# Optimization experiments

Measured on AMD Instinct MI355X. Metric: run time of the kernel, lower is better.

The kernel has to match this reference:

```python
import jax, jax.numpy as jnp
import numpy as np

T = 0.07          # cfg.CAP.TEMP
K = 50            # cfg.CAP.HARD_NEG_K
LOSS_WEIGHT = 0.5 # cfg.CAP.LOSS_WEIGHT
C_CAM = 8         # number of cameras
P = 2048          # pseudo-ID classes per camera bank


def setup_inputs() -> dict:
    key = jax.random.key(0)
    k1, k2, k3, k4 = jax.random.split(key, 4)
    B, D = 256, 2048
    inputs = jax.random.normal(k1, (B, D), jnp.float32)
    labels = jax.random.randint(k2, (B,), 0, P)
    cams = jax.random.randint(k3, (B,), 0, C_CAM)
    tempV = jax.random.normal(k4, (C_CAM * P, D), jnp.float32)
    tempV = tempV / jnp.linalg.norm(tempV, axis=1, keepdims=True)  # memory rows are L2-normalized
    return {"inputs": inputs, "labels": labels, "cams": cams, "tempV": tempV}


def _seg_mean_sum(vals, cams):
    # original loops over unique cams: loss += mean(vals within cam); empty cams contribute 0
    sums = jax.ops.segment_sum(vals, cams, num_segments=C_CAM)
    cnts = jax.ops.segment_sum(jnp.ones_like(vals), cams, num_segments=C_CAM)
    return jnp.sum(jnp.where(cnts > 0, sums / jnp.maximum(cnts, 1.0), 0.0))


def reference(inputs, labels, cams, tempV):
    B = inputs.shape[0]
    # cfg.CAP.NORM_FEAT
    x = inputs / jnp.linalg.norm(inputs, axis=1, keepdims=True)

    # one fused matmul against the concatenated memory; per-camera banks are contiguous P-slices
    all_logits = x @ tempV.T                      # [B, C_CAM*P]
    logits3 = all_logits.reshape(B, C_CAM, P)

    # ---- intra-camera loss: logits against the sample's own camera bank ----
    percam = jnp.take_along_axis(logits3, cams[:, None, None], axis=1)[:, 0, :] / T  # [B, P]
    lse_i = jax.scipy.special.logsumexp(percam, axis=1)
    ce = lse_i - jnp.take_along_axis(percam, labels[:, None], axis=1)[:, 0]
    loss_intra = _seg_mean_sum(ce, cams)

    # ---- inter-camera loss with hard-negative mining ----
    rows = jnp.arange(B)[:, None]
    # each ID has one centroid in every camera bank: positions label + P*cam
    ori_ind = labels[:, None] + P * jnp.arange(C_CAM)[None, :]        # [B, C_CAM]
    sims = all_logits.at[rows, ori_ind].set(-10000.0)                 # mask positives
    _, sel_ind = jax.lax.top_k(sims, K)                               # hard negatives (== sort[-K:])
    ori_logits = jnp.take_along_axis(all_logits, ori_ind, axis=1) / T  # [B, C_CAM]
    sel_logits = jnp.take_along_axis(all_logits, sel_ind, axis=1) / T  # [B, K]
    cat = jnp.concatenate([ori_logits, sel_logits], axis=1)            # [B, C_CAM+K]
    lse_c = jax.scipy.special.logsumexp(cat, axis=1)
    # target = 1/len(ori) on positives, 0 on negatives -> lse - mean(positive logits)
    loss_k = lse_c - jnp.mean(ori_logits, axis=1)
    loss_inter = LOSS_WEIGHT * _seg_mean_sum(loss_k, cams)

    return (loss_intra, loss_inter)
```

## Files before the change

### kernel.cpp

```cpp
#include <hip/hip_runtime.h>
#include <hip/hip_bf16.h>

#define BATCH 256
#define DIM   2048
#define NMEM  16384
#define PCLS  2048
#define CCAM  8
#define KSEL  50
#define T_INV 14.285714285714285714f
#define NBIN  4096

typedef __bf16 bf16x8 __attribute__((ext_vector_type(8)));
typedef float  f32x4  __attribute__((ext_vector_type(4)));

static __device__ __forceinline__ unsigned int f2bf(float f) {
  unsigned int u = __float_as_uint(f);
  return (u + 0x7FFFu + ((u >> 16) & 1u)) >> 16;
}
static __device__ __forceinline__ unsigned int pk2(float lo, float hi) {
  return f2bf(lo) | (f2bf(hi) << 16);
}
static __device__ __forceinline__ int binof(float v) {
  float bf = fmaf(v, 1950.4762f, 2048.0f);
  bf = fminf(fmaxf(bf, 0.0f), 4095.0f);
  return (int)bf;
}

__global__ __launch_bounds__(256) void norm_cast_kernel(
    const float* __restrict__ in, unsigned short* __restrict__ xb) {
  __shared__ float red[256];
  const int b = blockIdx.x, t = threadIdx.x;
  const float4* row = (const float4*)(in + (size_t)b * DIM);
  float4 a0 = row[t];
  float4 a1 = row[t + 256];
  float ss = a0.x*a0.x + a0.y*a0.y + a0.z*a0.z + a0.w*a0.w
           + a1.x*a1.x + a1.y*a1.y + a1.z*a1.z + a1.w*a1.w;
  red[t] = ss; __syncthreads();
  for (int s = 128; s > 0; s >>= 1) { if (t < s) red[t] += red[t + s]; __syncthreads(); }
  const float rn = rsqrtf(red[0]);
  ushort4 o0, o1;
  o0.x = (unsigned short)f2bf(a0.x*rn); o0.y = (unsigned short)f2bf(a0.y*rn);
  o0.z = (unsigned short)f2bf(a0.z*rn); o0.w = (unsigned short)f2bf(a0.w*rn);
  o1.x = (unsigned short)f2bf(a1.x*rn); o1.y = (unsigned short)f2bf(a1.y*rn);
  o1.z = (unsigned short)f2bf(a1.z*rn); o1.w = (unsigned short)f2bf(a1.w*rn);
  *(ushort4*)&xb[(size_t)b * DIM + t * 4]         = o0;
  *(ushort4*)&xb[(size_t)b * DIM + (t + 256) * 4] = o1;
}

#define BM 128
#define BN 64
#define BK 64
#define LDT 72

__global__ __launch_bounds__(256, 2) void gemm_kernel(
    const unsigned short* __restrict__ X,
    const float* __restrict__ V,
    float* __restrict__ C) {
  __shared__ unsigned short As[BM * LDT];
  __shared__ unsigned short Bs[BN * LDT];
  const int t  = threadIdx.x;
  const int m0 = blockIdx.x * BM;
  const int n0 = blockIdx.y * BN;
  const int lane = t & 63;
  const int w    = t >> 6;
  const int wm   = (w >> 1) * 64;
  const int wn   = (w & 1) * 32;

  f32x4 acc[4][2];
#pragma unroll
  for (int i = 0; i < 4; i++)
#pragma unroll
    for (int j = 0; j < 2; j++) acc[i][j] = (f32x4){0.f, 0.f, 0.f, 0.f};

  const int sr = t >> 1;
  const int sh = (t & 1) * 32;
  const int rb = t >> 2;
  const int cb = (t & 3) * 16;
  const unsigned short* Xp = X + (size_t)(m0 + sr) * DIM + sh;
  const float*          Vp = V + (size_t)(n0 + rb) * DIM + cb;

  uint4  a0 = *(const uint4*)Xp;
  uint4  a1 = *(const uint4*)(Xp + 8);
  uint4  a2 = *(const uint4*)(Xp + 16);
  uint4  a3 = *(const uint4*)(Xp + 24);
  float4 b0 = *(const float4*)Vp;
  float4 b1 = *(const float4*)(Vp + 4);
  float4 b2 = *(const float4*)(Vp + 8);
  float4 b3 = *(const float4*)(Vp + 12);

  const int fr = lane & 15;
  const int fk = (lane >> 4) * 8;

  for (int k0 = 0; k0 < DIM; k0 += BK) {
    __syncthreads();
    *(uint4*)&As[sr * LDT + sh]      = a0;
    *(uint4*)&As[sr * LDT + sh + 8]  = a1;
    *(uint4*)&As[sr * LDT + sh + 16] = a2;
    *(uint4*)&As[sr * LDT + sh + 24] = a3;
    uint4 p0, p1;
    p0.x = pk2(b0.x, b0.y); p0.y = pk2(b0.z, b0.w);
    p0.z = pk2(b1.x, b1.y); p0.w = pk2(b1.z, b1.w);
    p1.x = pk2(b2.x, b2.y); p1.y = pk2(b2.z, b2.w);
    p1.z = pk2(b3.x, b3.y); p1.w = pk2(b3.z, b3.w);
    *(uint4*)&Bs[rb * LDT + cb]     = p0;
    *(uint4*)&Bs[rb * LDT + cb + 8] = p1;
    __syncthreads();

    if (k0 + BK < DIM) {
      a0 = *(const uint4*)(Xp + k0 + BK);
      a1 = *(const uint4*)(Xp + k0 + BK + 8);
      a2 = *(const uint4*)(Xp + k0 + BK + 16);
      a3 = *(const uint4*)(Xp + k0 + BK + 24);
      b0 = *(const float4*)(Vp + k0 + BK);
      b1 = *(const float4*)(Vp + k0 + BK + 4);
      b2 = *(const float4*)(Vp + k0 + BK + 8);
      b3 = *(const float4*)(Vp + k0 + BK + 12);
    }

#pragma unroll
    for (int kk = 0; kk < BK; kk += 32) {
      bf16x8 aF[4], bF[2];
#pragma unroll
      for (int i = 0; i < 4; i++)
        aF[i] = *(const bf16x8*)&As[(wm + i * 16 + fr) * LDT + kk + fk];
#pragma unroll
      for (int j = 0; j < 2; j++)
        bF[j] = *(const bf16x8*)&Bs[(wn + j * 16 + fr) * LDT + kk + fk];
#pragma unroll
      for (int i = 0; i < 4; i++)
#pragma unroll
        for (int j = 0; j < 2; j++)
          acc[i][j] = __builtin_amdgcn_mfma_f32_16x16x32_bf16(aF[i], bF[j], acc[i][j], 0, 0, 0);
    }
  }

  const int cr = (lane >> 4) * 4;
  const int cc = lane & 15;
#pragma unroll
  for (int i = 0; i < 4; i++)
#pragma unroll
    for (int j = 0; j < 2; j++)
#pragma unroll
      for (int r = 0; r < 4; r++)
        C[(size_t)(m0 + wm + i * 16 + cr + r) * NMEM + (n0 + wn + j * 16 + cc)] =
            acc[i][j][r];
}

__global__ __launch_bounds__(256) void row_loss_kernel(
    const float* __restrict__ logits,
    const int* __restrict__ labels, const int* __restrict__ cams,
    float* __restrict__ ce_out, float* __restrict__ lossk_out) {
  __shared__ float vals[NMEM];
  __shared__ int   hist[NBIN];
  __shared__ float red[256];
  __shared__ int   pint[256];
  __shared__ float bl[512];
  __shared__ int   bcount;
  __shared__ int   bstar_s, cabove_s;

  const int b = blockIdx.x, t = threadIdx.x;
  const float4* src = (const float4*)(logits + (size_t)b * NMEM);
#pragma unroll
  for (int i = 0; i < 16; i++) ((float4*)vals)[t + 256 * i] = src[t + 256 * i];
#pragma unroll
  for (int i = 0; i < NBIN / 256; i++) hist[t + 256 * i] = 0;
  if (t == 0) bcount = 0;
  const int cam = cams[b], label = labels[b];
  __syncthreads();

  const int s0 = cam * PCLS;
  float S = 0.f;
#pragma unroll
  for (int i = 0; i < 8; i++) S += __expf(vals[s0 + t + 256 * i] * T_INV);
  red[t] = S; __syncthreads();
  for (int s = 128; s > 0; s >>= 1) { if (t < s) red[t] += red[t + s]; __syncthreads(); }
  float ov[CCAM]; float sumo = 0.f;
  if (t == 0) {
    ce_out[b] = logf(red[0]) - vals[s0 + label] * T_INV;
#pragma unroll
    for (int c = 0; c < CCAM; c++) { ov[c] = vals[c * PCLS + label]; sumo += ov[c]; }
  }
  __syncthreads();
  if (t < CCAM) vals[t * PCLS + label] = -1e30f;
  __syncthreads();

#pragma unroll
  for (int i = 0; i < 64; i++) {
    int bin = binof(vals[t + 256 * i]);
    atomicAdd(&hist[bin], 1);
  }
  __syncthreads();

  int ps = 0;
#pragma unroll
  for (int i = 0; i < 16; i++) ps += hist[t * 16 + i];
  pint[t] = ps; __syncthreads();
  if (t == 0) {
    int cum = 0, bstar = 0, cab = 0;
    for (int tc = 255; tc >= 0; tc--) {
      if (cum + pint[tc] >= KSEL) {
        for (int bi = tc * 16 + 15; bi >= tc * 16; bi--) {
          int h = hist[bi];
          if (cum + h >= KSEL) { bstar = bi; cab = cum; break; }
          cum += h;
        }
        break;
      }
      cum += pint[tc];
    }
    bstar_s = bstar; cabove_s = cab;
  }
  __syncthreads();
  const int bstar = bstar_s;

  float S2 = 0.f;
#pragma unroll
  for (int i = 0; i < 64; i++) {
    float v = vals[t + 256 * i];
    int bin = binof(v);
    if (bin > bstar) S2 += __expf(v * T_INV);
    else if (bin == bstar) {
      int p = atomicAdd(&bcount, 1);
      if (p < 512) bl[p] = v;
    }
  }
  red[t] = S2; __syncthreads();
  for (int s = 128; s > 0; s >>= 1) { if (t < s) red[t] += red[t + s]; __syncthreads(); }

  if (t == 0) {
    float S2tot = red[0];
    int need = KSEL - cabove_s;
    int bc = min(bcount, 512);
    for (int r = 0; r < need; r++) {
      float mx = -1e30f; int mi = 0;
      for (int i = 0; i < bc; i++) if (bl[i] > mx) { mx = bl[i]; mi = i; }
      S2tot += __expf(mx * T_INV);
      bl[mi] = -1e30f;
    }
#pragma unroll
    for (int c = 0; c < CCAM; c++) S2tot += __expf(ov[c] * T_INV);
    lossk_out[b] = logf(S2tot) - (sumo * T_INV) * (1.0f / CCAM);
  }
}

__global__ __launch_bounds__(256) void finalize_kernel(
    const float* __restrict__ ce, const float* __restrict__ lossk,
    const int* __restrict__ cams, float* __restrict__ out) {
  __shared__ float ce_s[BATCH], lk_s[BATCH];
  __shared__ int   cam_s[BATCH];
  __shared__ float si[CCAM], sk[CCAM], cnt[CCAM];
  const int t = threadIdx.x;
  ce_s[t]  = ce[t];
  lk_s[t]  = lossk[t];
  cam_s[t] = cams[t];
  __syncthreads();
  if (t < CCAM) {
    float a = 0.f, b = 0.f; int n = 0;
    for (int i = 0; i < BATCH; i++) {
      if (cam_s[i] == t) { a += ce_s[i]; b += lk_s[i]; n++; }
    }
    si[t] = a; sk[t] = b; cnt[t] = (float)n;
  }
  __syncthreads();
  if (t == 0) {
    float li = 0.f, lk = 0.f;
    for (int c = 0; c < CCAM; c++) {
      if (cnt[c] > 0.f) { li += si[c] / cnt[c]; lk += sk[c] / cnt[c]; }
    }
    out[0] = li;
    out[1] = 0.5f * lk;
  }
}

extern "C" void kernel_launch(void* const* d_in, const int* in_sizes, int n_in,
                              void* d_out, int out_size, void* d_ws, size_t ws_size,
                              hipStream_t stream) {
  const float* inputs = (const float*)d_in[0];
  const int*   labels = (const int*)d_in[1];
  const int*   cams   = (const int*)d_in[2];
  const float* tempV  = (const float*)d_in[3];
  float* out = (float*)d_out;

  char* ws = (char*)d_ws;
  unsigned short* xb  = (unsigned short*)ws;
  float* logits       = (float*)(ws + (1u << 20));
  float* ce           = (float*)(ws + (1u << 20) + (16u << 20));
  float* lossk        = (float*)(ws + (1u << 20) + (16u << 20) + 1024);

  norm_cast_kernel<<<BATCH, 256, 0, stream>>>(inputs, xb);
  gemm_kernel<<<dim3(BATCH / BM, NMEM / BN), 256, 0, stream>>>(xb, tempV, logits);
  row_loss_kernel<<<BATCH, 256, 0, stream>>>(logits, labels, cams, ce, lossk);
  finalize_kernel<<<1, 256, 0, stream>>>(ce, lossk, cams, out);
}
```

Before: 270.4 us.

## Double-buffer GEMM shared-memory tiles with two register prefetch sets

Restructures the GEMM main loop to use two LDS buffers and two register staging sets. Global loads now run two tiles ahead, and LDS writes of the next tile overlap with MFMA compute on the current one. This leaves one barrier per tile instead of two. In exchange it doubles LDS use and raises register pressure, which can lower occupancy under launch_bounds(256,2).

```diff
diff --git a/kernel.cpp b/kernel.cpp
--- a/kernel.cpp
+++ b/kernel.cpp
@@ -51,13 +51,14 @@
 #define BN 64
 #define BK 64
 #define LDT 72
+#define NTILE (DIM / BK)
 
 __global__ __launch_bounds__(256, 2) void gemm_kernel(
     const unsigned short* __restrict__ X,
     const float* __restrict__ V,
     float* __restrict__ C) {
-  __shared__ unsigned short As[BM * LDT];
-  __shared__ unsigned short Bs[BN * LDT];
+  __shared__ unsigned short As[2][BM * LDT];
+  __shared__ unsigned short Bs[2][BN * LDT];
   const int t  = threadIdx.x;
   const int m0 = blockIdx.x * BM;
   const int n0 = blockIdx.y * BN;
@@ -79,58 +80,65 @@
   const unsigned short* Xp = X + (size_t)(m0 + sr) * DIM + sh;
   const float*          Vp = V + (size_t)(n0 + rb) * DIM + cb;
 
-  uint4  a0 = *(const uint4*)Xp;
-  uint4  a1 = *(const uint4*)(Xp + 8);
-  uint4  a2 = *(const uint4*)(Xp + 16);
-  uint4  a3 = *(const uint4*)(Xp + 24);
-  float4 b0 = *(const float4*)Vp;
-  float4 b1 = *(const float4*)(Vp + 4);
-  float4 b2 = *(const float4*)(Vp + 8);
-  float4 b3 = *(const float4*)(Vp + 12);
-
   const int fr = lane & 15;
   const int fk = (lane >> 4) * 8;
 
-  for (int k0 = 0; k0 < DIM; k0 += BK) {
-    __syncthreads();
-    *(uint4*)&As[sr * LDT + sh]      = a0;
-    *(uint4*)&As[sr * LDT + sh + 8]  = a1;
-    *(uint4*)&As[sr * LDT + sh + 16] = a2;
-    *(uint4*)&As[sr * LDT + sh + 24] = a3;
+  uint4  xa[2][4];
+  float4 vb[2][4];
+
+  auto loadset = [&](int set, int koff) {
+#pragma unroll
+    for (int q = 0; q < 4; q++) xa[set][q] = *(const uint4*)(Xp + koff + q * 8);
+#pragma unroll
+    for (int q = 0; q < 4; q++) vb[set][q] = *(const float4*)(Vp + koff + q * 4);
+  };
+  auto stage = [&](int set, int buf) {
+    *(uint4*)&As[buf][sr * LDT + sh]      = xa[set][0];
+    *(uint4*)&As[buf][sr * LDT + sh + 8]  = xa[set][1];
+    *(uint4*)&As[buf][sr * LDT + sh + 16] = xa[set][2];
+    *(uint4*)&As[buf][sr * LDT + sh + 24] = xa[set][3];
     uint4 p0, p1;
-    p0.x = pk2(b0.x, b0.y); p0.y = pk2(b0.z, b0.w);
-    p0.z = pk2(b1.x, b1.y); p0.w = pk2(b1.z, b1.w);
-    p1.x = pk2(b2.x, b2.y); p1.y = pk2(b2.z, b2.w);
-    p1.z = pk2(b3.x, b3.y); p1.w = pk2(b3.z, b3.w);
-    *(uint4*)&Bs[rb * LDT + cb]     = p0;
-    *(uint4*)&Bs[rb * LDT + cb + 8] = p1;
-    __syncthreads();
-
-    if (k0 + BK < DIM) {
-      a0 = *(const uint4*)(Xp + k0 + BK);
-      a1 = *(const uint4*)(Xp + k0 + BK + 8);
-      a2 = *(const uint4*)(Xp + k0 + BK + 16);
-      a3 = *(const uint4*)(Xp + k0 + BK + 24);
-      b0 = *(const float4*)(Vp + k0 + BK);
-      b1 = *(const float4*)(Vp + k0 + BK + 4);
-      b2 = *(const float4*)(Vp + k0 + BK + 8);
-      b3 = *(const float4*)(Vp + k0 + BK + 12);
-    }
-
+    p0.x = pk2(vb[set][0].x, vb[set][0].y); p0.y = pk2(vb[set][0].z, vb[set][0].w);
+    p0.z = pk2(vb[set][1].x, vb[set][1].y); p0.w = pk2(vb[set][1].z, vb[set][1].w);
+    p1.x = pk2(vb[set][2].x, vb[set][2].y); p1.y = pk2(vb[set][2].z, vb[set][2].w);
+    p1.z = pk2(vb[set][3].x, vb[set][3].y); p1.w = pk2(vb[set][3].z, vb[set][3].w);
+    *(uint4*)&Bs[buf][rb * LDT + cb]     = p0;
+    *(uint4*)&Bs[buf][rb * LDT + cb + 8] = p1;
+  };
+  auto compute = [&](int buf) {
 #pragma unroll
     for (int kk = 0; kk < BK; kk += 32) {
       bf16x8 aF[4], bF[2];
 #pragma unroll
       for (int i = 0; i < 4; i++)
-        aF[i] = *(const bf16x8*)&As[(wm + i * 16 + fr) * LDT + kk + fk];
+        aF[i] = *(const bf16x8*)&As[buf][(wm + i * 16 + fr) * LDT + kk + fk];
 #pragma unroll
       for (int j = 0; j < 2; j++)
-        bF[j] = *(const bf16x8*)&Bs[(wn + j * 16 + fr) * LDT + kk + fk];
+        bF[j] = *(const bf16x8*)&Bs[buf][(wn + j * 16 + fr) * LDT + kk + fk];
 #pragma unroll
       for (int i = 0; i < 4; i++)
 #pragma unroll
         for (int j = 0; j < 2; j++)
           acc[i][j] = __builtin_amdgcn_mfma_f32_16x16x32_bf16(aF[i], bF[j], acc[i][j], 0, 0, 0);
+    }
+  };
+
+  loadset(0, 0);
+  loadset(1, BK);
+  stage(0, 0);
+  __syncthreads();
+
+  for (int j = 0; j < NTILE / 2; j++) {
+    const int base = j * 2 * BK;
+    if (base + 2 * BK < DIM) loadset(0, base + 2 * BK);
+    compute(0);
+    stage(1, 1);
+    __syncthreads();
+    if (base + 3 * BK < DIM) loadset(1, base + 3 * BK);
+    compute(1);
+    if (base + 2 * BK < DIM) {
+      stage(0, 0);
+      __syncthreads();
     }
   }
 
```

After: 326.0 us. 20.6% more time.
